# Kernel tuning notes

Hardware: AMD Instinct MI355X
Metric: run time of the kernel (lower is better)

## Reference

```python
import jax, jax.numpy as jnp
import numpy as np

NUM_RELATIONS = 8
NUM_BASES = 4
IN_CH, HID, OUT_CH = 128, 64, 64
N_NODES, N_EDGES = 50000, 500000


def rgcn_conv(x, edge_src, edge_dst, edge_type, basis, comp, root, bias):
    """PyG RGCNConv with basis decomposition and per-relation mean aggregation.
    basis: [B, in, out], comp: [R, B], root: [in, out], bias: [out].
    W_r = sum_b comp[r, b] * basis[b]; msg_e = x[src_e] @ W_{type_e};
    aggregate mean over incoming edges per (node, relation), sum over relations,
    then add root transform and bias.
    """
    n = x.shape[0]
    out_dim = basis.shape[2]
    # Project once through all bases: [N, B, out]  (cheap: B=4)
    h = jnp.einsum('ni,bio->nbo', x, basis)
    # Per-edge message: contract gathered basis features with per-edge comp coeffs
    msg = jnp.einsum('eb,ebo->eo', comp[edge_type], h[edge_src])  # [E, out]
    # Mean aggregation per (dst, relation): segment id = dst*R + relation
    seg = edge_dst * NUM_RELATIONS + edge_type
    sums = jax.ops.segment_sum(msg, seg, num_segments=n * NUM_RELATIONS)
    cnt = jax.ops.segment_sum(jnp.ones((msg.shape[0], 1), msg.dtype), seg,
                              num_segments=n * NUM_RELATIONS)
    mean = sums / jnp.maximum(cnt, 1.0)
    agg = mean.reshape(n, NUM_RELATIONS, out_dim).sum(axis=1)
    return agg + x @ root + bias


def setup_inputs() -> dict:
    key = jax.random.key(0)
    ks = jax.random.split(key, 12)
    s1 = 1.0 / np.sqrt(IN_CH)
    s2 = 1.0 / np.sqrt(HID)
    return {
        'x': jax.random.normal(ks[0], (N_NODES, IN_CH), jnp.float32),
        'edge_index': jax.random.randint(ks[1], (2, N_EDGES), 0, N_NODES, jnp.int64),
        'edge_type': jax.random.randint(ks[2], (N_EDGES,), 0, NUM_RELATIONS, jnp.int64),
        'basis1': jax.random.normal(ks[3], (NUM_BASES, IN_CH, HID), jnp.float32) * s1,
        'comp1': jax.random.normal(ks[4], (NUM_RELATIONS, NUM_BASES), jnp.float32) * 0.5,
        'root1': jax.random.normal(ks[5], (IN_CH, HID), jnp.float32) * s1,
        'bias1': jnp.zeros((HID,), jnp.float32),
        'basis2': jax.random.normal(ks[6], (NUM_BASES, HID, OUT_CH), jnp.float32) * s2,
        'comp2': jax.random.normal(ks[7], (NUM_RELATIONS, NUM_BASES), jnp.float32) * 0.5,
        'root2': jax.random.normal(ks[8], (HID, OUT_CH), jnp.float32) * s2,
        'bias2': jnp.zeros((OUT_CH,), jnp.float32),
    }


def reference(x, edge_index, edge_type, basis1, comp1, root1, bias1,
              basis2, comp2, root2, bias2):
    src, dst = edge_index[0], edge_index[1]
    h = rgcn_conv(x, src, dst, edge_type, basis1, comp1, root1, bias1)
    h = jax.nn.relu(h)
    out = rgcn_conv(h, src, dst, edge_type, basis2, comp2, root2, bias2)
    return out
```

## Files before the change

### kernel.cpp

```cpp
#include <hip/hip_runtime.h>
#include <cstddef>

#define NREL 8
#define SCAN_TILE 4096

typedef __bf16 bf16x8 __attribute__((ext_vector_type(8)));
typedef float f32x4 __attribute__((ext_vector_type(4)));

__device__ __forceinline__ unsigned f2bf_u(float f) {
    unsigned u = __float_as_uint(f);
    u += 0x7FFFu + ((u >> 16) & 1u);
    return u >> 16;
}
__device__ __forceinline__ short f2bf(float f) { return (short)f2bf_u(f); }
__device__ __forceinline__ int pack2bf(float lo, float hi) {
    return (int)(f2bf_u(lo) | (f2bf_u(hi) << 16));
}
__device__ __forceinline__ float bfval(unsigned short g) {
    return __uint_as_float((unsigned)g << 16);
}

__global__ __launch_bounds__(256) void hist_kernel(const int* __restrict__ dst,
                                                   const int* __restrict__ et,
                                                   int* __restrict__ cnt8, int E)
{
    int e = blockIdx.x * 256 + threadIdx.x;
    if (e < E) atomicAdd(&cnt8[dst[e] * NREL + et[e]], 1);
}

__global__ __launch_bounds__(256) void scan_part(const int* __restrict__ cnt8,
                                                 int* __restrict__ tsum, int n)
{
    int base = blockIdx.x * SCAN_TILE;
    int s = 0;
    for (int i = threadIdx.x; i < SCAN_TILE; i += 256) {
        int idx = base + i;
        if (idx < n) {
            int4 a = ((const int4*)cnt8)[idx * 2];
            int4 b = ((const int4*)cnt8)[idx * 2 + 1];
            s += a.x + a.y + a.z + a.w + b.x + b.y + b.z + b.w;
        }
    }
    for (int d = 1; d < 64; d <<= 1) s += __shfl_xor(s, d, 64);
    __shared__ int ws[4];
    if ((threadIdx.x & 63) == 0) ws[threadIdx.x >> 6] = s;
    __syncthreads();
    if (threadIdx.x == 0) tsum[blockIdx.x] = ws[0] + ws[1] + ws[2] + ws[3];
}

__global__ void scan_mid(int* __restrict__ tsum, int* __restrict__ offs_n, int nt)
{
    if (threadIdx.x == 0) {
        int run = 0;
        for (int i = 0; i < nt; ++i) { int t = tsum[i]; tsum[i] = run; run += t; }
        *offs_n = run;
    }
}

__global__ __launch_bounds__(256) void scan_final(const int* __restrict__ cnt8,
                                                  const int* __restrict__ tsum,
                                                  int* __restrict__ offs, int n)
{
    const int lane = threadIdx.x & 63, wid = threadIdx.x >> 6;
    int base = blockIdx.x * SCAN_TILE + threadIdx.x * 16;
    int v[16]; int s = 0;
#pragma unroll
    for (int j = 0; j < 16; ++j) {
        int idx = base + j;
        int dv = 0;
        if (idx < n) {
            int4 a = ((const int4*)cnt8)[idx * 2];
            int4 b = ((const int4*)cnt8)[idx * 2 + 1];
            dv = a.x + a.y + a.z + a.w + b.x + b.y + b.z + b.w;
        }
        v[j] = dv; s += dv;
    }
    int inc = s;
    for (int d = 1; d < 64; d <<= 1) {
        int t = __shfl_up(inc, d, 64);
        if (lane >= d) inc += t;
    }
    __shared__ int wsum[4];
    if (lane == 63) wsum[wid] = inc;
    __syncthreads();
    int run = tsum[blockIdx.x] + (inc - s);
    for (int k = 0; k < wid; ++k) run += wsum[k];
#pragma unroll
    for (int j = 0; j < 16; ++j) {
        int idx = base + j;
        if (idx < n) offs[idx] = run;
        run += v[j];
    }
}

__global__ __launch_bounds__(256) void scatter_kernel(const int* __restrict__ src,
                                                      const int* __restrict__ dst,
                                                      const int* __restrict__ et,
                                                      const int* __restrict__ offs,
                                                      int* __restrict__ cursor,
                                                      const int* __restrict__ cnt8,
                                                      int2* __restrict__ edgeP, int E)
{
    int e = blockIdx.x * 256 + threadIdx.x;
    if (e >= E) return;
    int d = dst[e], r = et[e], s = src[e];
    int c = cnt8[d * NREL + r];
    float inv = 1.0f / (float)(c > 1 ? c : 1);
    int pos = offs[d] + atomicAdd(&cursor[d], 1);
    edgeP[pos] = make_int2(s * NREL + r, __float_as_int(inv));
}

template<int K>
__global__ __launch_bounds__(256) void wfrag_kernel(const float* __restrict__ basis,
                                                    const float* __restrict__ root,
                                                    const float* __restrict__ comp,
                                                    short* __restrict__ Wf)
{
    constexpr int NK = K / 32;
    int tid = blockIdx.x * 256 + threadIdx.x;
    if (tid >= 36 * NK * 64) return;
    int lane = tid & 63, slot = tid >> 6;
    int ks = slot % NK, t = slot / NK;
    int kg = lane >> 4, lr = lane & 15;
    int k0 = ks * 32 + kg * 8;
    union { short s[8]; int4 v; } u;
#pragma unroll
    for (int e = 0; e < 8; ++e) {
        int k = k0 + e;
        float v;
        if (t < 32) {
            int rr = t >> 2, ch = (t & 3) * 16 + lr;
            v = comp[rr * 4 + 0] * basis[((size_t)0 * K + k) * 64 + ch]
              + comp[rr * 4 + 1] * basis[((size_t)1 * K + k) * 64 + ch]
              + comp[rr * 4 + 2] * basis[((size_t)2 * K + k) * 64 + ch]
              + comp[rr * 4 + 3] * basis[((size_t)3 * K + k) * 64 + ch];
        } else {
            v = root[(size_t)k * 64 + (t - 32) * 16 + lr];
        }
        u.s[e] = f2bf(v);
    }
    *(int4*)(Wf + (size_t)tid * 8) = u.v;
}

template<int K, bool AF32>
__global__ __launch_bounds__(256, 1) void gemm_mfma(const void* __restrict__ Ap,
                                                    const short* __restrict__ Wf,
                                                    const float* __restrict__ bias,
                                                    short* __restrict__ hr,
                                                    float* __restrict__ yinit, int N)
{
    constexpr int NK = K / 32;
    constexpr int CH = 9;
    __shared__ short lds[CH * NK * 512];

    const int w = threadIdx.x >> 6, lane = threadIdx.x & 63;
    const int kg = lane >> 4, lr = lane & 15;
    const int rt = blockIdx.x * 4 + w;

    bf16x8 afrag[NK];
    if (AF32) {
        const float* A = (const float*)Ap;
        int arow = rt * 16 + lr;
        int ar = arow < N ? arow : N - 1;
#pragma unroll
        for (int ks = 0; ks < NK; ++ks) {
            const float* ap = A + (size_t)ar * K + ks * 32 + kg * 8;
            float4 a = *(const float4*)ap;
            float4 b = *(const float4*)(ap + 4);
            union { short s[8]; bf16x8 v; } cv;
            cv.s[0] = f2bf(a.x); cv.s[1] = f2bf(a.y); cv.s[2] = f2bf(a.z); cv.s[3] = f2bf(a.w);
            cv.s[4] = f2bf(b.x); cv.s[5] = f2bf(b.y); cv.s[6] = f2bf(b.z); cv.s[7] = f2bf(b.w);
            afrag[ks] = cv.v;
        }
    } else {
        const short* A = (const short*)Ap;
        const short* ap = A + ((size_t)rt * NK * 64 + lane) * 8;
#pragma unroll
        for (int ks = 0; ks < NK; ++ks)
            afrag[ks] = *(const bf16x8*)(ap + ks * 512);
    }

    f32x4 acc[36];
#pragma unroll
    for (int t = 0; t < 36; ++t) acc[t] = (f32x4){0.f, 0.f, 0.f, 0.f};

    for (int c = 0; c < 4; ++c) {
        const int4* gsrc = (const int4*)(Wf + (size_t)c * CH * NK * 512);
        int4* ldst = (int4*)lds;
        for (int i = threadIdx.x; i < CH * NK * 64; i += 256)
            ldst[i] = gsrc[i];
        __syncthreads();
#pragma unroll
        for (int tt = 0; tt < CH; ++tt) {
#pragma unroll
            for (int ks = 0; ks < NK; ++ks) {
                bf16x8 bfrag = *(const bf16x8*)(lds + (tt * NK + ks) * 512 + lane * 8);
                acc[c * CH + tt] = __builtin_amdgcn_mfma_f32_16x16x32_bf16(
                    afrag[ks], bfrag, acc[c * CH + tt], 0, 0, 0);
            }
        }
        __syncthreads();
    }

    float b0 = bias[lr], b1 = bias[16 + lr], b2 = bias[32 + lr], b3 = bias[48 + lr];

    const int drow0 = rt * 16 + kg * 4;
#pragma unroll
    for (int r = 0; r < 4; ++r) {
        int dr = drow0 + r;
        if (dr >= N) break;
#pragma unroll
        for (int rr = 0; rr < 8; ++rr) {
            int u0 = pack2bf(acc[rr * 4 + 0][r], acc[rr * 4 + 1][r]);
            int u1 = pack2bf(acc[rr * 4 + 2][r], acc[rr * 4 + 3][r]);
            *(int2*)(hr + (size_t)dr * 512 + rr * 64 + lr * 4) = make_int2(u0, u1);
        }
        float4 o = make_float4(acc[32][r] + b0, acc[33][r] + b1,
                               acc[34][r] + b2, acc[35][r] + b3);
        *(float4*)(yinit + (size_t)dr * 64 + lr * 4) = o;
    }
}

template<bool BF16OUT>
__global__ __launch_bounds__(256) void agg_kernel(const int* __restrict__ offs,
                                                  const int2* __restrict__ edgeP,
                                                  const short* __restrict__ hr,
                                                  const float* __restrict__ init,
                                                  float* __restrict__ outF,
                                                  short* __restrict__ outB, int N)
{
    const int dst = blockIdx.x * 4 + (threadIdx.x >> 6);
    const int l = threadIdx.x & 63;
    if (dst >= N) return;

    const unsigned short* hp = (const unsigned short*)hr;
    float acc = init[(size_t)dst * 64 + l];
    int e0 = offs[dst], e1 = offs[dst + 1];

    int e = e0;
    for (; e + 3 < e1; e += 4) {
        int2 p0 = edgeP[e],     p1 = edgeP[e + 1];
        int2 p2 = edgeP[e + 2], p3 = edgeP[e + 3];
        unsigned short g0 = hp[(size_t)p0.x * 64 + l];
        unsigned short g1 = hp[(size_t)p1.x * 64 + l];
        unsigned short g2 = hp[(size_t)p2.x * 64 + l];
        unsigned short g3 = hp[(size_t)p3.x * 64 + l];
        acc = fmaf(bfval(g0), __int_as_float(p0.y), acc);
        acc = fmaf(bfval(g1), __int_as_float(p1.y), acc);
        acc = fmaf(bfval(g2), __int_as_float(p2.y), acc);
        acc = fmaf(bfval(g3), __int_as_float(p3.y), acc);
    }
    for (; e < e1; ++e) {
        int2 p0 = edgeP[e];
        unsigned short g0 = hp[(size_t)p0.x * 64 + l];
        acc = fmaf(bfval(g0), __int_as_float(p0.y), acc);
    }

    int tc = (l & 3) * 16 + (l >> 2);
    if (BF16OUT) {
        int rt2 = dst >> 4, lr2 = dst & 15;
        int ks2 = tc >> 5, kg2 = (tc >> 3) & 3, e2 = tc & 7;
        outB[(((size_t)rt2 * 2 + ks2) * 64 + kg2 * 16 + lr2) * 8 + e2] =
            f2bf(fmaxf(acc, 0.f));
    } else {
        outF[(size_t)dst * 64 + tc] = acc;
    }
}

extern "C" void kernel_launch(void* const* d_in, const int* in_sizes, int n_in,
                              void* d_out, int out_size, void* d_ws, size_t ws_size,
                              hipStream_t stream)
{
    const float* x      = (const float*)d_in[0];
    const int*   ei     = (const int*)d_in[1];
    const int*   et     = (const int*)d_in[2];
    const float* basis1 = (const float*)d_in[3];
    const float* comp1  = (const float*)d_in[4];
    const float* root1  = (const float*)d_in[5];
    const float* bias1  = (const float*)d_in[6];
    const float* basis2 = (const float*)d_in[7];
    const float* comp2  = (const float*)d_in[8];
    const float* root2  = (const float*)d_in[9];
    const float* bias2  = (const float*)d_in[10];
    float* out = (float*)d_out;

    const int N = in_sizes[0] / 128;
    const int E = in_sizes[2];
    const int* src  = ei;
    const int* dstp = ei + E;

    const int gblk = (N + 63) / 64;
    const int NT   = gblk * 4;
    const int ablk = (N + 3) / 4;

    char* p = (char*)d_ws;
    auto carve = [&](size_t bytes) -> char* {
        char* q = p; p += (bytes + 255) & ~(size_t)255; return q;
    };
    int*   cursor  = (int*)carve((size_t)N * 4);
    int*   cnt8    = (int*)carve((size_t)N * NREL * 4);
    char*  zend    = p;
    int*   offs    = (int*)carve((size_t)(N + 1) * 4);
    int*   tsum    = (int*)carve(256 * 4);
    int2*  edgeP   = (int2*)carve((size_t)E * 8);
    short* Wf1     = (short*)carve((size_t)36 * 4 * 64 * 8 * 2);
    short* Wf2     = (short*)carve((size_t)36 * 2 * 64 * 8 * 2);
    float* yinit   = (float*)carve((size_t)N * 64 * 4);
    short* xf2     = (short*)carve((size_t)NT * 2 * 64 * 8 * 2);
    short* hr      = (short*)carve((size_t)N * 512 * 2);

    hipMemsetAsync(cursor, 0, (size_t)(zend - (char*)cursor), stream);

    const int ntiles = (N + SCAN_TILE - 1) / SCAN_TILE;

    hist_kernel<<<(E + 255) / 256, 256, 0, stream>>>(dstp, et, cnt8, E);
    scan_part<<<ntiles, 256, 0, stream>>>(cnt8, tsum, N);
    scan_mid<<<1, 64, 0, stream>>>(tsum, offs + N, ntiles);
    scan_final<<<ntiles, 256, 0, stream>>>(cnt8, tsum, offs, N);
    scatter_kernel<<<(E + 255) / 256, 256, 0, stream>>>(src, dstp, et, offs, cursor,
                                                        cnt8, edgeP, E);

    wfrag_kernel<128><<<(36 * 4 * 64 + 255) / 256, 256, 0, stream>>>(basis1, root1, comp1, Wf1);
    wfrag_kernel<64><<<(36 * 2 * 64 + 255) / 256, 256, 0, stream>>>(basis2, root2, comp2, Wf2);

    gemm_mfma<128, true><<<gblk, 256, 0, stream>>>(x, Wf1, bias1, hr, yinit, N);
    agg_kernel<true><<<ablk, 256, 0, stream>>>(offs, edgeP, hr, yinit, nullptr, xf2, N);

    gemm_mfma<64, false><<<gblk, 256, 0, stream>>>(xf2, Wf2, bias2, hr, yinit, N);
    agg_kernel<false><<<ablk, 256, 0, stream>>>(offs, edgeP, hr, yinit, out, nullptr, N);
}
```

Measured before the change: 205.5 us.

## Split GEMM output columns across grid y and read weights directly from global

The fused GEMM is split across a second grid dimension so each block computes 12 of the 36 output tiles (3 groups of 64 columns) instead of all 36. The LDS staging of weight fragments and its barriers are removed, and B fragments are loaded straight from global/L2. This cuts accumulator registers from 36 to 12 tiles and drops the min-1-block launch bound, which should raise occupancy. In exchange the A rows are reloaded (and converted from fp32 for layer 1) three times, and weight reads now go through cache rather than shared memory.

New measurement: 200.2 us. 2.6% less time.

```diff
diff --git a/kernel.cpp b/kernel.cpp
--- a/kernel.cpp
+++ b/kernel.cpp
@@ -143,19 +143,17 @@
 }
 
 template<int K, bool AF32>
-__global__ __launch_bounds__(256, 1) void gemm_mfma(const void* __restrict__ Ap,
-                                                    const short* __restrict__ Wf,
-                                                    const float* __restrict__ bias,
-                                                    short* __restrict__ hr,
-                                                    float* __restrict__ yinit, int N)
+__global__ __launch_bounds__(256) void gemm_mfma(const void* __restrict__ Ap,
+                                                 const short* __restrict__ Wf,
+                                                 const float* __restrict__ bias,
+                                                 short* __restrict__ hr,
+                                                 float* __restrict__ yinit, int N)
 {
     constexpr int NK = K / 32;
-    constexpr int CH = 9;
-    __shared__ short lds[CH * NK * 512];
-
     const int w = threadIdx.x >> 6, lane = threadIdx.x & 63;
     const int kg = lane >> 4, lr = lane & 15;
     const int rt = blockIdx.x * 4 + w;
+    const int g0 = blockIdx.y * 3;
 
     bf16x8 afrag[NK];
     if (AF32) {
@@ -180,26 +178,19 @@
             afrag[ks] = *(const bf16x8*)(ap + ks * 512);
     }
 
-    f32x4 acc[36];
-#pragma unroll
-    for (int t = 0; t < 36; ++t) acc[t] = (f32x4){0.f, 0.f, 0.f, 0.f};
-
-    for (int c = 0; c < 4; ++c) {
-        const int4* gsrc = (const int4*)(Wf + (size_t)c * CH * NK * 512);
-        int4* ldst = (int4*)lds;
-        for (int i = threadIdx.x; i < CH * NK * 64; i += 256)
-            ldst[i] = gsrc[i];
-        __syncthreads();
-#pragma unroll
-        for (int tt = 0; tt < CH; ++tt) {
-#pragma unroll
-            for (int ks = 0; ks < NK; ++ks) {
-                bf16x8 bfrag = *(const bf16x8*)(lds + (tt * NK + ks) * 512 + lane * 8);
-                acc[c * CH + tt] = __builtin_amdgcn_mfma_f32_16x16x32_bf16(
-                    afrag[ks], bfrag, acc[c * CH + tt], 0, 0, 0);
-            }
-        }
-        __syncthreads();
+    f32x4 acc[12];
+#pragma unroll
+    for (int t = 0; t < 12; ++t) acc[t] = (f32x4){0.f, 0.f, 0.f, 0.f};
+
+    const short* bp = Wf + ((size_t)g0 * 4 * NK * 64 + lane) * 8;
+#pragma unroll
+    for (int tt = 0; tt < 12; ++tt) {
+#pragma unroll
+        for (int ks = 0; ks < NK; ++ks) {
+            bf16x8 bfrag = *(const bf16x8*)(bp + (size_t)(tt * NK + ks) * 512);
+            acc[tt] = __builtin_amdgcn_mfma_f32_16x16x32_bf16(afrag[ks], bfrag,
+                                                              acc[tt], 0, 0, 0);
+        }
     }
 
     float b0 = bias[lr], b1 = bias[16 + lr], b2 = bias[32 + lr], b3 = bias[48 + lr];
@@ -210,14 +201,18 @@
         int dr = drow0 + r;
         if (dr >= N) break;
 #pragma unroll
-        for (int rr = 0; rr < 8; ++rr) {
-            int u0 = pack2bf(acc[rr * 4 + 0][r], acc[rr * 4 + 1][r]);
-            int u1 = pack2bf(acc[rr * 4 + 2][r], acc[rr * 4 + 3][r]);
-            *(int2*)(hr + (size_t)dr * 512 + rr * 64 + lr * 4) = make_int2(u0, u1);
-        }
-        float4 o = make_float4(acc[32][r] + b0, acc[33][r] + b1,
-                               acc[34][r] + b2, acc[35][r] + b3);
-        *(float4*)(yinit + (size_t)dr * 64 + lr * 4) = o;
+        for (int gg = 0; gg < 3; ++gg) {
+            int g = g0 + gg;
+            if (g < 8) {
+                int u0 = pack2bf(acc[gg * 4 + 0][r], acc[gg * 4 + 1][r]);
+                int u1 = pack2bf(acc[gg * 4 + 2][r], acc[gg * 4 + 3][r]);
+                *(int2*)(hr + (size_t)dr * 512 + g * 64 + lr * 4) = make_int2(u0, u1);
+            } else {
+                float4 o = make_float4(acc[gg * 4 + 0][r] + b0, acc[gg * 4 + 1][r] + b1,
+                                       acc[gg * 4 + 2][r] + b2, acc[gg * 4 + 3][r] + b3);
+                *(float4*)(yinit + (size_t)dr * 64 + lr * 4) = o;
+            }
+        }
     }
 }
 
@@ -323,9 +318,9 @@
     wfrag_kernel<128><<<(36 * 4 * 64 + 255) / 256, 256, 0, stream>>>(basis1, root1, comp1, Wf1);
     wfrag_kernel<64><<<(36 * 2 * 64 + 255) / 256, 256, 0, stream>>>(basis2, root2, comp2, Wf2);
 
-    gemm_mfma<128, true><<<gblk, 256, 0, stream>>>(x, Wf1, bias1, hr, yinit, N);
+    gemm_mfma<128, true><<<dim3(gblk, 3), 256, 0, stream>>>(x, Wf1, bias1, hr, yinit, N);
     agg_kernel<true><<<ablk, 256, 0, stream>>>(offs, edgeP, hr, yinit, nullptr, xf2, N);
 
-    gemm_mfma<64, false><<<gblk, 256, 0, stream>>>(xf2, Wf2, bias2, hr, yinit, N);
+    gemm_mfma<64, false><<<dim3(gblk, 3), 256, 0, stream>>>(xf2, Wf2, bias2, hr, yinit, N);
     agg_kernel<false><<<ablk, 256, 0, stream>>>(offs, edgeP, hr, yinit, out, nullptr, N);
 }
```
